# Kernel tuning notes

Hardware: AMD Instinct MI355X
Metric: run time of the kernel (lower is better)

The kernel has to match this reference:

```python
import jax, jax.numpy as jnp
import numpy as np

B, T, K, H = 2, 2048, 1024, 16


def setup_inputs() -> dict:
    key = jax.random.key(0)
    ks = jax.random.split(key, 9)
    sc = 0.02
    return {
        "x": jax.random.normal(ks[0], (B, T, K), dtype=jnp.float32),
        "Wq_w": jax.random.normal(ks[1], (K, K), dtype=jnp.float32) * sc,
        "Wq_b": jax.random.normal(ks[2], (K,), dtype=jnp.float32) * sc,
        "Wk_w": jax.random.normal(ks[3], (K, K), dtype=jnp.float32) * sc,
        "Wk_b": jax.random.normal(ks[4], (K,), dtype=jnp.float32) * sc,
        "Wv_w": jax.random.normal(ks[5], (K, K), dtype=jnp.float32) * sc,
        "Wv_b": jax.random.normal(ks[6], (K,), dtype=jnp.float32) * sc,
        "Wo_w": jax.random.normal(ks[7], (K, K), dtype=jnp.float32) * sc,
        "Wo_b": jax.random.normal(ks[8], (K,), dtype=jnp.float32) * sc,
    }


def reference(x, Wq_w, Wq_b, Wk_w, Wk_b, Wv_w, Wv_b, Wo_w, Wo_b):
    b, t, k = x.shape
    h = H
    s = k // h
    # nn.Linear: y = x @ W^T + b
    q = x @ Wq_w.T + Wq_b
    kk = x @ Wk_w.T + Wk_b
    v = x @ Wv_w.T + Wv_b
    # [b, t, h, s] -> [b, h, t, s]
    q = q.reshape(b, t, h, s).transpose(0, 2, 1, 3)
    kk = kk.reshape(b, t, h, s).transpose(0, 2, 1, 3)
    v = v.reshape(b, t, h, s).transpose(0, 2, 1, 3)
    # scores [b, h, t, t]
    dot = jnp.einsum("bhqd,bhkd->bhqk", q, kk)
    # causal mask: upper triangle (offset=1) set to -inf BEFORE scaling
    causal = jnp.tril(jnp.ones((t, t), dtype=bool))
    dot = jnp.where(causal, dot, -jnp.inf)
    # NOTE: original scales by sqrt(k) (full model dim), not sqrt(head_dim)
    dot = dot / jnp.sqrt(jnp.asarray(k, dot.dtype))
    attn = jax.nn.softmax(dot, axis=-1)
    out = jnp.einsum("bhqk,bhkd->bhqd", attn, v)  # [b, h, t, s]
    out = out.transpose(0, 2, 1, 3).reshape(b, t, k)
    return out @ Wo_w.T + Wo_b
```

## Files before the change

kernel.cpp:

```cpp
#include <hip/hip_runtime.h>

typedef unsigned short u16;
typedef unsigned int u32;
typedef __bf16 bf16x8 __attribute__((ext_vector_type(8)));
typedef float f32x4 __attribute__((ext_vector_type(4)));
typedef unsigned short u16x8 __attribute__((ext_vector_type(8)));
typedef unsigned int u32x4 __attribute__((ext_vector_type(4)));

#define B_ 2
#define T_ 2048
#define K_ 1024
#define H_ 16
#define S_ 64
#define MKC 4194304
#define QSCALE 0.04508422f

__device__ __forceinline__ u16 f2bf(float f) {
  unsigned int u = __builtin_bit_cast(unsigned int, f);
  u += 0x7fffu + ((u >> 16) & 1u);
  return (u16)(u >> 16);
}

__device__ __forceinline__ f32x4 MFMA(bf16x8 a, bf16x8 b, f32x4 c) {
  return __builtin_amdgcn_mfma_f32_16x16x32_bf16(a, b, c, 0, 0, 0);
}

__device__ __forceinline__ void gld16(const void* g, void* l) {
  __builtin_amdgcn_global_load_lds((const __attribute__((address_space(1))) void*)g,
                                   (__attribute__((address_space(3))) void*)l, 16, 0, 0);
}

template <int N>
__device__ __forceinline__ void waitv() {
  asm volatile("s_waitcnt vmcnt(%0)" ::"i"(N) : "memory");
}
__device__ __forceinline__ void memfence_barrier() {
  asm volatile("" ::: "memory");
  __builtin_amdgcn_s_barrier();
}

__global__ __launch_bounds__(256) void cvt_all(const float* __restrict__ x,
                                               const float* __restrict__ W0,
                                               const float* __restrict__ W1,
                                               const float* __restrict__ W2,
                                               const float* __restrict__ W3,
                                               u16* __restrict__ xb,
                                               u16* __restrict__ wb) {
  const int i = blockIdx.x * 256 + threadIdx.x;
  const float* src;
  u16* dst;
  if (i < 524288) {
    src = x + (size_t)i * 8;
    dst = xb + (size_t)i * 8;
  } else {
    const int j = i - 524288;
    const int sel = j >> 17;
    const float* W = sel == 0 ? W0 : sel == 1 ? W1 : sel == 2 ? W2 : W3;
    src = W + (size_t)(j & 131071) * 8;
    dst = wb + (size_t)j * 8;
  }
  const float4* s = (const float4*)src;
  float4 f0 = s[0], f1 = s[1];
  u16x8 p;
  p[0] = f2bf(f0.x); p[1] = f2bf(f0.y); p[2] = f2bf(f0.z); p[3] = f2bf(f0.w);
  p[4] = f2bf(f1.x); p[5] = f2bf(f1.y); p[6] = f2bf(f1.z); p[7] = f2bf(f1.w);
  *(u16x8*)dst = p;
}

template <int OMODE, int BN>
__global__ __launch_bounds__(256) void gemm16(const u16* __restrict__ A,
                                              const u16* __restrict__ Bm,
                                              const float* __restrict__ b0,
                                              const float* __restrict__ b1,
                                              const float* __restrict__ b2,
                                              void* __restrict__ C0,
                                              int M, int N, int K) {
  constexpr int NF = BN / 32;
  constexpr int SOPS = 2 + BN / 64;
  __shared__ u16 As[2][128 * 32];
  __shared__ u16 Bs[2][BN * 32];
  const int bm = blockIdx.x * 128;
  const int bn = blockIdx.y * BN;
  const int tid = threadIdx.x;
  const int w = tid >> 6, lane = tid & 63;
  const int wr = (w >> 1) * 64, wc = (w & 1) * (BN / 2);
  const int lr = lane & 15, g = lane >> 4;
  const int lk = (g ^ ((lr >> 1) & 3)) * 8;
  const int srow = lane >> 2;
  const int scol = ((lane & 3) ^ ((lane >> 3) & 3)) * 8;

  f32x4 acc[4][NF] = {};

  auto stg = [&](int buf, int k0) {
#pragma unroll
    for (int i = 0; i < 2; ++i) {
      const int rbase = (i * 4 + w) * 16;
      gld16(A + (size_t)(bm + rbase + srow) * K + k0 + scol, &As[buf][rbase * 32]);
    }
#pragma unroll
    for (int i = 0; i < BN / 64; ++i) {
      const int rbase = (i * 4 + w) * 16;
      gld16(Bm + (size_t)(bn + rbase + srow) * K + k0 + scol, &Bs[buf][rbase * 32]);
    }
  };

  stg(0, 0);
  const int NK = K >> 5;
  for (int kk = 0; kk < NK; ++kk) {
    const int buf = kk & 1;
    const bool pf = (kk + 1 < NK);
    if (pf) {
      stg(buf ^ 1, (kk + 1) * 32);
      waitv<SOPS>();
    } else {
      waitv<0>();
    }
    __builtin_amdgcn_s_barrier();
    bf16x8 af[4], bfr[NF];
#pragma unroll
    for (int m = 0; m < 4; ++m)
      af[m] = *(const bf16x8*)&As[buf][(wr + m * 16 + lr) * 32 + lk];
#pragma unroll
    for (int n = 0; n < NF; ++n)
      bfr[n] = *(const bf16x8*)&Bs[buf][(wc + n * 16 + lr) * 32 + lk];
#pragma unroll
    for (int m = 0; m < 4; ++m)
#pragma unroll
      for (int n = 0; n < NF; ++n)
        acc[m][n] = MFMA(af[m], bfr[n], acc[m][n]);
    memfence_barrier();
  }

  const int sel = (OMODE == 2) ? 0 : (bn >> 10);
  const float* bp = (OMODE == 2) ? b0 : (sel == 0 ? b0 : sel == 1 ? b1 : b2);
#pragma unroll
  for (int n = 0; n < NF; ++n) {
    const int col = bn + wc + n * 16 + lr;
    const float bv = bp[(OMODE == 2) ? col : (col & 1023)];
#pragma unroll
    for (int m = 0; m < 4; ++m) {
#pragma unroll
      for (int r = 0; r < 4; ++r) {
        const int row = bm + wr + m * 16 + g * 4 + r;
        float v = acc[m][n][r] + bv;
        if (OMODE == 2) {
          ((float*)C0)[(size_t)row * N + col] = v;
        } else {
          u16* dst = (u16*)C0;
          const int cc = col & 1023;
          if (sel == 2) {
            const int bb = row >> 11, t = row & 2047, hh = cc >> 6, ss = cc & 63;
            dst[(size_t)2 * MKC + (((size_t)(bb * H_ + hh) * S_ + ss) << 11) + t] = f2bf(v);
          } else {
            if (sel == 0) v *= QSCALE;
            dst[(size_t)sel * MKC + (size_t)row * 1024 + cc] = f2bf(v);
          }
        }
      }
    }
  }
}

__global__ __launch_bounds__(256) void attn_fwd(const u16* __restrict__ Q,
                                                const u16* __restrict__ Kb,
                                                const u16* __restrict__ Vt,
                                                u16* __restrict__ O) {
  __shared__ u16 Ks[2][64 * 64];
  __shared__ u16 Vs[2][64 * 64];
  const int tid = threadIdx.x;
  const int w = tid >> 6, lane = tid & 63;
  const int qh = lane & 15;
  const int g = lane >> 4;
  const int bh = blockIdx.x;
  const int b = bh >> 4, h = bh & 15;
  const int yy = blockIdx.y;
  const int y = (yy < 8) ? yy : 23 - yy;
  const int nkA = y + 1, nkB = y + 17;
  const int qwA = y * 64 + w * 16;
  const int qwB = (y + 16) * 64 + w * 16;
  const int myqA = qwA + qh, myqB = qwB + qh;

  const size_t qoffA = (size_t)(b * T_ + qwA + qh) * K_ + h * S_ + g * 8;
  const bf16x8 bqA0 = *(const bf16x8*)(Q + qoffA);
  const bf16x8 bqA1 = *(const bf16x8*)(Q + qoffA + 32);
  const size_t qoffB = (size_t)(b * T_ + qwB + qh) * K_ + h * S_ + g * 8;
  const bf16x8 bqB0 = *(const bf16x8*)(Q + qoffB);
  const bf16x8 bqB1 = *(const bf16x8*)(Q + qoffB + 32);

  const int srow = lane >> 3;
  const int sl8 = ((lane & 7) ^ srow) * 8;
  int kvp[2];
#pragma unroll
  for (int i = 0; i < 2; ++i) {
    const int rho = w * 16 + i * 8 + srow;
    const int a = rho >> 4;
    kvp[i] = ((a >> 1) << 5) | (((rho >> 2) & 3) << 3) | ((a & 1) << 2) | (rho & 3);
  }
  const int ksw = qh & 7;
  u16x8 ov;
#pragma unroll
  for (int i = 0; i < 8; ++i) ov[i] = 0x3F80;
  const bf16x8 ones = __builtin_bit_cast(bf16x8, ov);

  const u16* kq0 = Kb + (size_t)(b * T_ + kvp[0]) * K_ + h * S_ + sl8;
  const u16* kq1 = Kb + (size_t)(b * T_ + kvp[1]) * K_ + h * S_ + sl8;
  const u16* vq0 = Vt + (size_t)(bh * S_ + w * 16 + srow) * T_ + sl8;
  const u16* vq1 = Vt + (size_t)(bh * S_ + w * 16 + 8 + srow) * T_ + sl8;

  auto stage = [&](int buf) {
    gld16(kq0, &Ks[buf][(w * 16) * 64]);
    gld16(kq1, &Ks[buf][(w * 16 + 8) * 64]);
    gld16(vq0, &Vs[buf][(w * 16) * 64]);
    gld16(vq1, &Vs[buf][(w * 16 + 8) * 64]);
    kq0 += 64 * K_; kq1 += 64 * K_; vq0 += 64; vq1 += 64;
  };

  f32x4 oA[4] = {}, oB[4] = {};
  f32x4 olA = {}, olB = {};

  auto QKT = [&](int buf, f32x4 (&sO)[4], bf16x8 q0, bf16x8 q1) {
    __builtin_amdgcn_s_setprio(1);
#pragma unroll
    for (int a = 0; a < 4; ++a) {
      const u16* kr = &Ks[buf][(a * 16 + qh) * 64];
      const bf16x8 kf0 = *(const bf16x8*)(kr + ((g ^ ksw) * 8));
      const bf16x8 kf1 = *(const bf16x8*)(kr + (((4 + g) ^ ksw) * 8));
      f32x4 z = {0.f, 0.f, 0.f, 0.f};
      z = MFMA(kf0, q0, z);
      sO[a] = MFMA(kf1, q1, z);
    }
    __builtin_amdgcn_s_setprio(0);
  };

  auto SMPV = [&](f32x4 (&sIn)[4], int buf, int k0, int qw, int myq,
                  f32x4 (&o)[4], f32x4& ol) {
    float p[4][4];
    if (k0 + 63 > qw) {
      const int thr = myq - k0 - (g << 3);
#pragma unroll
      for (int a = 0; a < 4; ++a)
#pragma unroll
        for (int r = 0; r < 4; ++r) {
          const int C = ((a >> 1) << 5) + ((a & 1) << 2) + r;
          p[a][r] = (C <= thr) ? __builtin_amdgcn_exp2f(sIn[a][r]) : 0.f;
        }
    } else {
#pragma unroll
      for (int a = 0; a < 4; ++a)
#pragma unroll
        for (int r = 0; r < 4; ++r)
          p[a][r] = __builtin_amdgcn_exp2f(sIn[a][r]);
    }

    __builtin_amdgcn_s_setprio(1);
#pragma unroll
    for (int c = 0; c < 2; ++c) {
      u32 t0, t1, t2, t3;
      asm("v_cvt_pk_bf16_f32 %0, %1, %2" : "=v"(t0) : "v"(p[2 * c][0]), "v"(p[2 * c][1]));
      asm("v_cvt_pk_bf16_f32 %0, %1, %2" : "=v"(t1) : "v"(p[2 * c][2]), "v"(p[2 * c][3]));
      asm("v_cvt_pk_bf16_f32 %0, %1, %2" : "=v"(t2) : "v"(p[2 * c + 1][0]), "v"(p[2 * c + 1][1]));
      asm("v_cvt_pk_bf16_f32 %0, %1, %2" : "=v"(t3) : "v"(p[2 * c + 1][2]), "v"(p[2 * c + 1][3]));
      u32x4 tv; tv[0] = t0; tv[1] = t1; tv[2] = t2; tv[3] = t3;
      const bf16x8 pa = __builtin_bit_cast(bf16x8, tv);
      ol = MFMA(pa, ones, ol);
#pragma unroll
      for (int nn = 0; nn < 4; ++nn) {
        const bf16x8 vf =
            *(const bf16x8*)(&Vs[buf][(16 * nn + qh) * 64] + (((c * 4 + g) ^ ksw) * 8));
        o[nn] = MFMA(pa, vf, o[nn]);
      }
    }
    __builtin_amdgcn_s_setprio(0);
  };

  stage(0);
  for (int kt = 0; kt < nkB; ++kt) {
    const int cur = kt & 1;
    const bool hn = kt + 1 < nkB;
    if (hn) {
      stage(cur ^ 1);
      waitv<4>();
    } else {
      waitv<0>();
    }
    __builtin_amdgcn_s_barrier();

    if (kt < nkA) {
      f32x4 s4[4];
      QKT(cur, s4, bqA0, bqA1);
      SMPV(s4, cur, kt * 64, qwA, myqA, oA, olA);
    }
    {
      f32x4 s4[4];
      QKT(cur, s4, bqB0, bqB1);
      SMPV(s4, cur, kt * 64, qwB, myqB, oB, olB);
    }

    memfence_barrier();
  }

#pragma unroll
  for (int r = 0; r < 4; ++r) {
    const float invA = 1.f / olA[r];
    const size_t rowA = (size_t)(b * T_ + qwA + 4 * g + r);
#pragma unroll
    for (int nn = 0; nn < 4; ++nn)
      O[rowA * K_ + h * S_ + nn * 16 + qh] = f2bf(oA[nn][r] * invA);
    const float invB = 1.f / olB[r];
    const size_t rowB = (size_t)(b * T_ + qwB + 4 * g + r);
#pragma unroll
    for (int nn = 0; nn < 4; ++nn)
      O[rowB * K_ + h * S_ + nn * 16 + qh] = f2bf(oB[nn][r] * invB);
  }
}

extern "C" void kernel_launch(void* const* d_in, const int* in_sizes, int n_in,
                              void* d_out, int out_size, void* d_ws, size_t ws_size,
                              hipStream_t stream) {
  (void)in_sizes; (void)n_in; (void)out_size; (void)ws_size;
  const float* x  = (const float*)d_in[0];
  const float* Wq = (const float*)d_in[1];
  const float* bq = (const float*)d_in[2];
  const float* Wk = (const float*)d_in[3];
  const float* bk = (const float*)d_in[4];
  const float* Wv = (const float*)d_in[5];
  const float* bv = (const float*)d_in[6];
  const float* Wo = (const float*)d_in[7];
  const float* bo = (const float*)d_in[8];
  float* out = (float*)d_out;

  const size_t MK = (size_t)MKC;
  const size_t WK = (size_t)K_ * K_;
  u16* Qb  = (u16*)d_ws;
  u16* Kbf = Qb + MK;
  u16* Vtb = Kbf + MK;
  u16* AO  = Vtb + MK;
  u16* xb  = AO + MK;
  u16* Wqkv = xb + MK;
  u16* Wob  = Wqkv + 3 * WK;

  dim3 blk(256);
  cvt_all<<<dim3(4096), blk, 0, stream>>>(x, Wq, Wk, Wv, Wo, xb, Wqkv);
  gemm16<3, 128><<<dim3(32, 24), blk, 0, stream>>>(xb, Wqkv, bq, bk, bv, Qb,
                                                   B_ * T_, 3 * K_, K_);
  attn_fwd<<<dim3(B_ * H_, 16), blk, 0, stream>>>(Qb, Kbf, Vtb, AO);
  gemm16<2, 64><<<dim3(32, 16), blk, 0, stream>>>(AO, Wob, bo, bo, bo, out,
                                                  B_ * T_, K_, K_);
}
```

Before: 105.6 us.

## Switch attention kernel to 32x32x16 MFMA with 128-row query blocks

Rewrites the attention inner loop to use 32x32x16 bf16 MFMA instead of 16x16x32. Each wave now owns 32 query rows of one contiguous 128-row block, replacing the earlier scheme where each block paired a light and a heavy 64-row tile for causal load balancing. K staging order, LDS fragment indexing, the causal mask and the output layout are remapped to the 32x32 accumulator layout. The aim is fewer LDS reads per FLOP and larger MFMA tiles. The cost is uneven per-block work along the causal diagonal and more accumulator registers per wave.

```diff
diff --git a/kernel.cpp b/kernel.cpp
--- a/kernel.cpp
+++ b/kernel.cpp
@@ -4,8 +4,8 @@
 typedef unsigned int u32;
 typedef __bf16 bf16x8 __attribute__((ext_vector_type(8)));
 typedef float f32x4 __attribute__((ext_vector_type(4)));
+typedef float f32x16 __attribute__((ext_vector_type(16)));
 typedef unsigned short u16x8 __attribute__((ext_vector_type(8)));
-typedef unsigned int u32x4 __attribute__((ext_vector_type(4)));
 
 #define B_ 2
 #define T_ 2048
@@ -23,6 +23,9 @@
 
 __device__ __forceinline__ f32x4 MFMA(bf16x8 a, bf16x8 b, f32x4 c) {
   return __builtin_amdgcn_mfma_f32_16x16x32_bf16(a, b, c, 0, 0, 0);
+}
+__device__ __forceinline__ f32x16 MFMA32(bf16x8 a, bf16x8 b, f32x16 c) {
+  return __builtin_amdgcn_mfma_f32_32x32x16_bf16(a, b, c, 0, 0, 0);
 }
 
 __device__ __forceinline__ void gld16(const void* g, void* l) {
@@ -169,41 +172,38 @@
   __shared__ u16 Vs[2][64 * 64];
   const int tid = threadIdx.x;
   const int w = tid >> 6, lane = tid & 63;
-  const int qh = lane & 15;
-  const int g = lane >> 4;
+  const int q5 = lane & 31;
+  const int g1 = lane >> 5;
+  const int l7 = lane & 7;
   const int bh = blockIdx.x;
   const int b = bh >> 4, h = bh & 15;
   const int yy = blockIdx.y;
   const int y = (yy < 8) ? yy : 23 - yy;
-  const int nkA = y + 1, nkB = y + 17;
-  const int qwA = y * 64 + w * 16;
-  const int qwB = (y + 16) * 64 + w * 16;
-  const int myqA = qwA + qh, myqB = qwB + qh;
-
-  const size_t qoffA = (size_t)(b * T_ + qwA + qh) * K_ + h * S_ + g * 8;
-  const bf16x8 bqA0 = *(const bf16x8*)(Q + qoffA);
-  const bf16x8 bqA1 = *(const bf16x8*)(Q + qoffA + 32);
-  const size_t qoffB = (size_t)(b * T_ + qwB + qh) * K_ + h * S_ + g * 8;
-  const bf16x8 bqB0 = *(const bf16x8*)(Q + qoffB);
-  const bf16x8 bqB1 = *(const bf16x8*)(Q + qoffB + 32);
+  const int qb = y * 128;
+  const int qw = qb + 32 * w;
+  const int nk = 2 * y + 2;
+
+  bf16x8 bq[4];
+  const size_t qoff = (size_t)(b * T_ + qw + q5) * K_ + h * S_ + g1 * 8;
+#pragma unroll
+  for (int j = 0; j < 4; ++j) bq[j] = *(const bf16x8*)(Q + qoff + j * 16);
 
   const int srow = lane >> 3;
   const int sl8 = ((lane & 7) ^ srow) * 8;
-  int kvp[2];
+  int ksrc[2];
 #pragma unroll
   for (int i = 0; i < 2; ++i) {
     const int rho = w * 16 + i * 8 + srow;
-    const int a = rho >> 4;
-    kvp[i] = ((a >> 1) << 5) | (((rho >> 2) & 3) << 3) | ((a & 1) << 2) | (rho & 3);
-  }
-  const int ksw = qh & 7;
+    const int j = rho & 3, g1b = (rho >> 2) & 1, v = (rho >> 3) & 1, u = (rho >> 4) & 1;
+    ksrc[i] = (rho & 32) + 16 * v + 8 * g1b + 4 * u + j;
+  }
   u16x8 ov;
 #pragma unroll
   for (int i = 0; i < 8; ++i) ov[i] = 0x3F80;
   const bf16x8 ones = __builtin_bit_cast(bf16x8, ov);
 
-  const u16* kq0 = Kb + (size_t)(b * T_ + kvp[0]) * K_ + h * S_ + sl8;
-  const u16* kq1 = Kb + (size_t)(b * T_ + kvp[1]) * K_ + h * S_ + sl8;
+  const u16* kq0 = Kb + (size_t)(b * T_ + ksrc[0]) * K_ + h * S_ + sl8;
+  const u16* kq1 = Kb + (size_t)(b * T_ + ksrc[1]) * K_ + h * S_ + sl8;
   const u16* vq0 = Vt + (size_t)(bh * S_ + w * 16 + srow) * T_ + sl8;
   const u16* vq1 = Vt + (size_t)(bh * S_ + w * 16 + 8 + srow) * T_ + sl8;
 
@@ -215,68 +215,12 @@
     kq0 += 64 * K_; kq1 += 64 * K_; vq0 += 64; vq1 += 64;
   };
 
-  f32x4 oA[4] = {}, oB[4] = {};
-  f32x4 olA = {}, olB = {};
-
-  auto QKT = [&](int buf, f32x4 (&sO)[4], bf16x8 q0, bf16x8 q1) {
-    __builtin_amdgcn_s_setprio(1);
-#pragma unroll
-    for (int a = 0; a < 4; ++a) {
-      const u16* kr = &Ks[buf][(a * 16 + qh) * 64];
-      const bf16x8 kf0 = *(const bf16x8*)(kr + ((g ^ ksw) * 8));
-      const bf16x8 kf1 = *(const bf16x8*)(kr + (((4 + g) ^ ksw) * 8));
-      f32x4 z = {0.f, 0.f, 0.f, 0.f};
-      z = MFMA(kf0, q0, z);
-      sO[a] = MFMA(kf1, q1, z);
-    }
-    __builtin_amdgcn_s_setprio(0);
-  };
-
-  auto SMPV = [&](f32x4 (&sIn)[4], int buf, int k0, int qw, int myq,
-                  f32x4 (&o)[4], f32x4& ol) {
-    float p[4][4];
-    if (k0 + 63 > qw) {
-      const int thr = myq - k0 - (g << 3);
-#pragma unroll
-      for (int a = 0; a < 4; ++a)
-#pragma unroll
-        for (int r = 0; r < 4; ++r) {
-          const int C = ((a >> 1) << 5) + ((a & 1) << 2) + r;
-          p[a][r] = (C <= thr) ? __builtin_amdgcn_exp2f(sIn[a][r]) : 0.f;
-        }
-    } else {
-#pragma unroll
-      for (int a = 0; a < 4; ++a)
-#pragma unroll
-        for (int r = 0; r < 4; ++r)
-          p[a][r] = __builtin_amdgcn_exp2f(sIn[a][r]);
-    }
-
-    __builtin_amdgcn_s_setprio(1);
-#pragma unroll
-    for (int c = 0; c < 2; ++c) {
-      u32 t0, t1, t2, t3;
-      asm("v_cvt_pk_bf16_f32 %0, %1, %2" : "=v"(t0) : "v"(p[2 * c][0]), "v"(p[2 * c][1]));
-      asm("v_cvt_pk_bf16_f32 %0, %1, %2" : "=v"(t1) : "v"(p[2 * c][2]), "v"(p[2 * c][3]));
-      asm("v_cvt_pk_bf16_f32 %0, %1, %2" : "=v"(t2) : "v"(p[2 * c + 1][0]), "v"(p[2 * c + 1][1]));
-      asm("v_cvt_pk_bf16_f32 %0, %1, %2" : "=v"(t3) : "v"(p[2 * c + 1][2]), "v"(p[2 * c + 1][3]));
-      u32x4 tv; tv[0] = t0; tv[1] = t1; tv[2] = t2; tv[3] = t3;
-      const bf16x8 pa = __builtin_bit_cast(bf16x8, tv);
-      ol = MFMA(pa, ones, ol);
-#pragma unroll
-      for (int nn = 0; nn < 4; ++nn) {
-        const bf16x8 vf =
-            *(const bf16x8*)(&Vs[buf][(16 * nn + qh) * 64] + (((c * 4 + g) ^ ksw) * 8));
-        o[nn] = MFMA(pa, vf, o[nn]);
-      }
-    }
-    __builtin_amdgcn_s_setprio(0);
-  };
+  f32x16 o0 = {}, o1 = {}, ol = {};
 
   stage(0);
-  for (int kt = 0; kt < nkB; ++kt) {
+  for (int kt = 0; kt < nk; ++kt) {
     const int cur = kt & 1;
-    const bool hn = kt + 1 < nkB;
+    const bool hn = kt + 1 < nk;
     if (hn) {
       stage(cur ^ 1);
       waitv<4>();
@@ -285,32 +229,74 @@
     }
     __builtin_amdgcn_s_barrier();
 
-    if (kt < nkA) {
-      f32x4 s4[4];
-      QKT(cur, s4, bqA0, bqA1);
-      SMPV(s4, cur, kt * 64, qwA, myqA, oA, olA);
-    }
-    {
-      f32x4 s4[4];
-      QKT(cur, s4, bqB0, bqB1);
-      SMPV(s4, cur, kt * 64, qwB, myqB, oB, olB);
-    }
+    f32x16 sT[2];
+    __builtin_amdgcn_s_setprio(1);
+#pragma unroll
+    for (int kh = 0; kh < 2; ++kh) {
+      f32x16 acc = {};
+#pragma unroll
+      for (int j = 0; j < 4; ++j) {
+        const bf16x8 kf = *(const bf16x8*)
+            &Ks[cur][(kh * 32 + q5) * 64 + (((j * 2 + g1) ^ l7) * 8)];
+        acc = MFMA32(kf, bq[j], acc);
+      }
+      sT[kh] = acc;
+    }
+    __builtin_amdgcn_s_setprio(0);
+
+    const int k0 = kt * 64;
+    bf16x8 pa[2][2];
+#pragma unroll
+    for (int kh = 0; kh < 2; ++kh) {
+      float p[16];
+      if (k0 + 63 > qw) {
+        const int lim = qw + q5 - k0 - kh * 32 - g1 * 8;
+#pragma unroll
+        for (int r = 0; r < 16; ++r) {
+          const int C = 16 * ((r >> 2) & 1) + 4 * (r >> 3) + (r & 3);
+          p[r] = (C <= lim) ? __builtin_amdgcn_exp2f(sT[kh][r]) : 0.f;
+        }
+      } else {
+#pragma unroll
+        for (int r = 0; r < 16; ++r)
+          p[r] = __builtin_amdgcn_exp2f(sT[kh][r]);
+      }
+#pragma unroll
+      for (int c = 0; c < 2; ++c) {
+        u32 t0, t1, t2, t3;
+        asm("v_cvt_pk_bf16_f32 %0, %1, %2" : "=v"(t0) : "v"(p[4 * c]), "v"(p[4 * c + 1]));
+        asm("v_cvt_pk_bf16_f32 %0, %1, %2" : "=v"(t1) : "v"(p[4 * c + 2]), "v"(p[4 * c + 3]));
+        asm("v_cvt_pk_bf16_f32 %0, %1, %2" : "=v"(t2) : "v"(p[4 * c + 8]), "v"(p[4 * c + 9]));
+        asm("v_cvt_pk_bf16_f32 %0, %1, %2" : "=v"(t3) : "v"(p[4 * c + 10]), "v"(p[4 * c + 11]));
+        u32 tv[4] = {t0, t1, t2, t3};
+        pa[kh][c] = __builtin_bit_cast(bf16x8, *(ulonglong2*)tv);
+      }
+    }
+
+    __builtin_amdgcn_s_setprio(1);
+#pragma unroll
+    for (int kh = 0; kh < 2; ++kh)
+#pragma unroll
+      for (int c = 0; c < 2; ++c) {
+        const int slotb = kh * 4 + c * 2 + g1;
+        ol = MFMA32(pa[kh][c], ones, ol);
+        const bf16x8 vf0 = *(const bf16x8*)&Vs[cur][q5 * 64 + ((slotb ^ l7) * 8)];
+        o0 = MFMA32(pa[kh][c], vf0, o0);
+        const bf16x8 vf1 = *(const bf16x8*)&Vs[cur][(32 + q5) * 64 + (((slotb ^ (l7))) * 8)];
+        o1 = MFMA32(pa[kh][c], vf1, o1);
+      }
+    __builtin_amdgcn_s_setprio(0);
 
     memfence_barrier();
   }
 
 #pragma unroll
-  for (int r = 0; r < 4; ++r) {
-    const float invA = 1.f / olA[r];
-    const size_t rowA = (size_t)(b * T_ + qwA + 4 * g + r);
-#pragma unroll
-    for (int nn = 0; nn < 4; ++nn)
-      O[rowA * K_ + h * S_ + nn * 16 + qh] = f2bf(oA[nn][r] * invA);
-    const float invB = 1.f / olB[r];
-    const size_t rowB = (size_t)(b * T_ + qwB + 4 * g + r);
-#pragma unroll
-    for (int nn = 0; nn < 4; ++nn)
-      O[rowB * K_ + h * S_ + nn * 16 + qh] = f2bf(oB[nn][r] * invB);
+  for (int r = 0; r < 16; ++r) {
+    const float inv = 1.f / ol[r];
+    const int qrow = qw + (r & 3) + 8 * (r >> 2) + 4 * g1;
+    const size_t base = (size_t)(b * T_ + qrow) * K_ + h * S_ + q5;
+    O[base] = f2bf(o0[r] * inv);
+    O[base + 32] = f2bf(o1[r] * inv);
   }
 }
 
```

Result: slower. 111.8 us (+5.9%).
